# Kernel tuning notes

Hardware: AMD Instinct MI355X
Metric: run time of the kernel (lower is better)

The kernel has to match this reference:

```python
import jax, jax.numpy as jnp
import numpy as np

EPS = 1e-3  # Keras BatchNormalization default epsilon


def _bn_params(key, c):
    k1, k2, k3, k4 = jax.random.split(key, 4)
    gamma = 1.0 + 0.1 * jax.random.normal(k1, (c,), jnp.float32)
    beta = 0.1 * jax.random.normal(k2, (c,), jnp.float32)
    mean = 0.1 * jax.random.normal(k3, (c,), jnp.float32)
    var = 0.5 + jax.random.uniform(k4, (c,), jnp.float32)
    return jnp.stack([gamma, beta, mean, var])  # (4, c)


def bn(x, p):
    g, b, m, v = p[0], p[1], p[2], p[3]
    return (x - m) * jax.lax.rsqrt(v + EPS) * g + b


def setup_inputs() -> dict:
    key = jax.random.key(0)
    ks = jax.random.split(key, 32)
    B, N, C, K = 32, 2048, 3, 32
    MLP1, UNITS = 128, 512
    w = lambda k, shp, fan: jax.random.normal(k, shp, jnp.float32) / np.sqrt(fan)
    inp = {
        "inputs": jax.random.normal(ks[0], (B, N, C), jnp.float32),
        "indices": jax.random.randint(ks[1], (B, N, K), 0, N, jnp.int32),
        "t_conv1_w": w(ks[2], (C, 64), C), "t_conv1_b": 0.1 * jax.random.normal(ks[3], (64,), jnp.float32),
        "t_bn1": _bn_params(ks[4], 64),
        "t_dense1_w": w(ks[5], (64, 64), 64), "t_dense1_b": 0.1 * jax.random.normal(ks[6], (64,), jnp.float32),
        "t_bn2": _bn_params(ks[7], 64),
        "t_dense2_w": w(ks[8], (64, C * C), 64), "t_dense2_b": 0.1 * jax.random.normal(ks[9], (C * C,), jnp.float32),
        "conv1_w": w(ks[10], (K * C, MLP1), K * C), "conv1_b": 0.1 * jax.random.normal(ks[11], (MLP1,), jnp.float32),
        "bn1": _bn_params(ks[12], MLP1),
        "conv2_w": w(ks[13], (MLP1, 2 * MLP1), MLP1), "conv2_b": 0.1 * jax.random.normal(ks[14], (2 * MLP1,), jnp.float32),
        "bn2": _bn_params(ks[15], 2 * MLP1),
        "bn3": _bn_params(ks[16], 2 * MLP1),
        "dense1_w": w(ks[17], (2 * MLP1, C), 2 * MLP1), "dense1_b": 0.1 * jax.random.normal(ks[18], (C,), jnp.float32),
        "conv3_w": w(ks[19], (C, UNITS), C), "conv3_b": 0.1 * jax.random.normal(ks[20], (UNITS,), jnp.float32),
        "bn4": _bn_params(ks[21], UNITS),
        "blk1_w": w(ks[22], (UNITS, UNITS // 2), UNITS), "blk1_b": 0.1 * jax.random.normal(ks[23], (UNITS // 2,), jnp.float32),
        "blk1_bn": _bn_params(ks[24], UNITS // 2),
        "blk2_w": w(ks[25], (UNITS // 2, UNITS // 4), UNITS // 2), "blk2_b": 0.1 * jax.random.normal(ks[26], (UNITS // 4,), jnp.float32),
        "blk2_bn": _bn_params(ks[27], UNITS // 4),
        "bn_globf": _bn_params(ks[28], UNITS // 4),
    }
    return inp


def reference(inputs, indices, t_conv1_w, t_conv1_b, t_bn1, t_dense1_w, t_dense1_b,
              t_bn2, t_dense2_w, t_dense2_b, conv1_w, conv1_b, bn1, conv2_w, conv2_b,
              bn2, bn3, dense1_w, dense1_b, conv3_w, conv3_b, bn4,
              blk1_w, blk1_b, blk1_bn, blk2_w, blk2_b, blk2_bn, bn_globf):
    B, N, C = inputs.shape
    # --- TNetLess (inference: dropout = identity) ---
    x = jax.nn.relu(bn(inputs @ t_conv1_w + t_conv1_b, t_bn1))   # (B,N,64)
    x = jnp.max(x, axis=1)                                        # global max pool -> (B,64)
    x = jax.nn.relu(bn(x @ t_dense1_w + t_dense1_b, t_bn2))      # (B,64)
    transform = (x @ t_dense2_w + t_dense2_b).reshape(B, C, C)   # (B,C,C)
    pct = jnp.einsum('bnc,bcd->bnd', inputs, transform)          # transformed cloud (B,N,C)
    # --- random neighbor gather (batch_dims=1) ---
    feats = pct[jnp.arange(B)[:, None, None], indices]           # (B,N,K,C)
    feats = feats.reshape(B, N, -1)                               # (B,N,K*C)
    # --- pointwise MLP over gathered neighbor features ---
    feats = jax.nn.relu(bn(feats @ conv1_w + conv1_b, bn1))      # (B,N,128)
    feats = jax.nn.relu(bn(feats @ conv2_w + conv2_b, bn2))      # (B,N,256)
    g = bn(jnp.max(feats, axis=1), bn3)                           # (B,256)
    g = jnp.broadcast_to(g[:, None, :], (B, N, g.shape[-1]))     # tile to (B,N,256)
    g = g @ dense1_w + dense1_b                                   # (B,N,C)
    combined = jnp.concatenate([pct, g], axis=1)                  # concat on point axis -> (B,2N,C)
    # --- conv3 + conv blocks (kernel_size=1 -> pointwise) ---
    net = jax.nn.relu(bn(combined @ conv3_w + conv3_b, bn4))     # (B,2N,512)
    net = jax.nn.relu(bn(net @ blk1_w + blk1_b, blk1_bn))        # (B,2N,256)
    net = jax.nn.relu(bn(net @ blk2_w + blk2_b, blk2_bn))        # (B,2N,128)
    net = jnp.max(net, axis=1)                                    # (B,128)
    return bn(net, bn_globf)
```

## Files before the change

### kernel.cpp

```cpp
#include <hip/hip_runtime.h>

typedef unsigned short u16;
typedef unsigned int u32;
typedef __attribute__((ext_vector_type(8))) short bf16x8;
typedef __attribute__((ext_vector_type(4))) float f32x4;

#define EPSBN 0.001f
#define MFMA16(a, b, c) __builtin_amdgcn_mfma_f32_16x16x32_bf16(a, b, c, 0, 0, 0)

__device__ __forceinline__ float bf2f(u16 u) {
    return __uint_as_float(((u32)u) << 16);
}
__device__ __forceinline__ u16 f2bf(float f) {
    u32 u = __float_as_uint(f);
    u32 r = u + 0x7FFFu + ((u >> 16) & 1u);
    return (u16)(r >> 16);
}
__device__ __forceinline__ float relu(float x) { return x > 0.f ? x : 0.f; }
__device__ __forceinline__ float rdv(const void* p, int i, int isbf) {
    return isbf ? bf2f(((const u16*)p)[i]) : ((const float*)p)[i];
}

#define A_INPUTS 64
#define A_TC1W  196672
#define A_TC1B  196864
#define A_TBN1  196928
#define A_TD1W  197184
#define A_TD1B  201280
#define A_TBN2  201344
#define A_TD2W  201600
#define A_TD2B  202176
#define A_BN3   249216
#define A_D1W   250240
#define A_D1B   251008
#define A_BNGF  420928
#define S_PCT   423808
#define S_MAXF  620544
#define S_NETMAX 628736
#define T_C1WT  634880
#define T_C2WT  641024
#define T_W4T   657408
#define T_W5T   722944
#define P_W3S   739328
#define P_B3S   740864
#define P_BP1   741376
#define P_BP2   741504
#define P_BP4   741760
#define P_BP5   742016

struct SmallCv { const void* src[12]; int n[12]; int off[12]; };
struct PrepWA { const void* src[4]; const void* bn[4]; int K[4]; int logN[4]; int base[4]; int dstoff[4]; };
struct PrepSm { const void *bn4, *c3w, *c3b, *bn2, *c2b, *blk1bn, *blk1b, *bn1, *c1b, *blk2bn, *blk2b; };

__global__ __launch_bounds__(256) void k_prep(SmallCv sc, PrepWA pw, PrepSm ps,
                                              const void* __restrict__ inputs_raw,
                                              const u16* __restrict__ tbn1_raw,
                                              float* __restrict__ ws) {
    __shared__ float tile[32][65];
    __shared__ float scol[64];
    int isbf = 1;
    for (int i = 0; i < 16; i += 2) {
        u16 v = tbn1_raw[i];
        if (v < 0x3E00u || v > 0x4080u) isbf = 0;
    }
    int bx = blockIdx.x, tid = threadIdx.x;
    if (bx < 32) {
        float* dst = ws + A_INPUTS;
        for (int i = bx * 256 + tid; i < 196608; i += 8192) dst[i] = rdv(inputs_raw, i, isbf);
    } else if (bx < 36) {
        int t0 = (bx - 32) * 3;
        for (int t = t0; t < t0 + 3; t++) {
            int n = sc.n[t];
            float* dst = ws + sc.off[t];
            for (int i = tid; i < n; i += 256) dst[i] = rdv(sc.src[t], i, isbf);
        }
    } else if (bx < 138) {
        int blk = bx - 36;
        int t = (blk < 6) ? 0 : (blk < 22) ? 1 : (blk < 86) ? 2 : 3;
        int tt = blk - pw.base[t];
        int N = 1 << pw.logN[t];
        int K = pw.K[t];
        int ct = N >> 6;
        int k0 = (tt / ct) * 32, c0 = (tt % ct) * 64;
        if (tid < 64) {
            int c = c0 + tid;
            scol[tid] = rdv(pw.bn[t], c, isbf) * rsqrtf(rdv(pw.bn[t], 3 * N + c, isbf) + EPSBN);
        }
        __syncthreads();
#pragma unroll
        for (int pr = 0; pr < 8; pr++) {
            int kr = pr * 4 + (tid >> 6), cc = tid & 63;
            tile[kr][cc] = rdv(pw.src[t], (k0 + kr) * N + c0 + cc, isbf) * scol[cc];
        }
        __syncthreads();
        u32* d32 = (u32*)((u16*)(ws + pw.dstoff[t]));
#pragma unroll
        for (int pw2 = 0; pw2 < 4; pw2++) {
            int cr = pw2 * 16 + (tid >> 4);
            int kp = tid & 15;
            u32 pk = (u32)f2bf(tile[kp * 2][cr]) | ((u32)f2bf(tile[kp * 2 + 1][cr]) << 16);
            d32[(((c0 + cr) * K + k0) >> 1) + kp] = pk;
        }
    } else if (bx == 138) {
        for (int c = tid; c < 512; c += 256) {
            float s = rdv(ps.bn4, c, isbf) * rsqrtf(rdv(ps.bn4, 1536 + c, isbf) + EPSBN);
            float t = rdv(ps.bn4, 512 + c, isbf) - rdv(ps.bn4, 1024 + c, isbf) * s;
            ws[P_W3S + c]        = rdv(ps.c3w, c, isbf) * s;
            ws[P_W3S + 512 + c]  = rdv(ps.c3w, 512 + c, isbf) * s;
            ws[P_W3S + 1024 + c] = rdv(ps.c3w, 1024 + c, isbf) * s;
            ws[P_B3S + c] = rdv(ps.c3b, c, isbf) * s + t;
        }
        {
            int c = tid;
            float s2 = rdv(ps.bn2, c, isbf) * rsqrtf(rdv(ps.bn2, 768 + c, isbf) + EPSBN);
            ws[P_BP2 + c] = rdv(ps.c2b, c, isbf) * s2 + (rdv(ps.bn2, 256 + c, isbf) - rdv(ps.bn2, 512 + c, isbf) * s2);
            float s5 = rdv(ps.blk1bn, c, isbf) * rsqrtf(rdv(ps.blk1bn, 768 + c, isbf) + EPSBN);
            ws[P_BP4 + c] = rdv(ps.blk1b, c, isbf) * s5 + (rdv(ps.blk1bn, 256 + c, isbf) - rdv(ps.blk1bn, 512 + c, isbf) * s5);
        }
        if (tid < 128) {
            int c = tid;
            float s1 = rdv(ps.bn1, c, isbf) * rsqrtf(rdv(ps.bn1, 384 + c, isbf) + EPSBN);
            ws[P_BP1 + c] = rdv(ps.c1b, c, isbf) * s1 + (rdv(ps.bn1, 128 + c, isbf) - rdv(ps.bn1, 256 + c, isbf) * s1);
            float s6 = rdv(ps.blk2bn, c, isbf) * rsqrtf(rdv(ps.blk2bn, 384 + c, isbf) + EPSBN);
            ws[P_BP5 + c] = rdv(ps.blk2b, c, isbf) * s6 + (rdv(ps.blk2bn, 128 + c, isbf) - rdv(ps.blk2bn, 256 + c, isbf) * s6);
        }
    } else {
        u32* z = (u32*)(ws + S_MAXF);
        for (int i = tid; i < 12288; i += 256) z[i] = 0u;
        if (tid == 0) ((u32*)ws)[0] = (u32)isbf;
    }
}

__global__ __launch_bounds__(256) void k_tnet(const float* __restrict__ inp,
                                              const float* __restrict__ w,
                                              const float* __restrict__ bias,
                                              const float* __restrict__ bn,
                                              const float* __restrict__ w1, const float* __restrict__ b1,
                                              const float* __restrict__ bn2p,
                                              const float* __restrict__ w2, const float* __restrict__ b2,
                                              float* __restrict__ pct) {
    __shared__ float pts[6144];
    __shared__ float wred[4][64];
    __shared__ float x1v[64];
    __shared__ float x2v[64];
    __shared__ float tf[9];
    int b = blockIdx.x, tid = threadIdx.x;
    const float* ip = inp + (size_t)b * 2048 * 3;
#pragma unroll
    for (int i = 0; i < 24; i++) pts[tid + i * 256] = ip[tid + i * 256];

    int c = tid & 63, pg = tid >> 6;
    float w0 = w[c], w1c = w[64 + c], w2c = w[128 + c], bi = bias[c];
    float g = bn[c], be = bn[64 + c], m = bn[128 + c], v = bn[192 + c];
    float s = g * rsqrtf(v + EPSBN), t = be - m * s;
    __syncthreads();

    float vmax = 0.f;
    int pbase = pg * 512;
#pragma unroll 4
    for (int p = 0; p < 512; p++) {
        float x0 = pts[(pbase + p) * 3], x1 = pts[(pbase + p) * 3 + 1], x2 = pts[(pbase + p) * 3 + 2];
        float z = x0 * w0 + x1 * w1c + x2 * w2c + bi;
        vmax = fmaxf(vmax, z * s + t);
    }
    wred[pg][c] = vmax;
    __syncthreads();
    if (tid < 64) {
        float mm = fmaxf(fmaxf(wred[0][tid], wred[1][tid]), fmaxf(wred[2][tid], wred[3][tid]));
        x1v[tid] = relu(mm);
    }
    __syncthreads();
    if (tid < 64) {
        float acc = b1[tid];
        for (int j = 0; j < 64; j++) acc += x1v[j] * w1[j * 64 + tid];
        float g2 = bn2p[tid], be2 = bn2p[64 + tid], m2 = bn2p[128 + tid], v2 = bn2p[192 + tid];
        float s2 = g2 * rsqrtf(v2 + EPSBN);
        x2v[tid] = relu(acc * s2 + (be2 - m2 * s2));
    }
    __syncthreads();
    if (tid < 9) {
        float a = b2[tid];
        for (int j = 0; j < 64; j++) a += x2v[j] * w2[j * 9 + tid];
        tf[tid] = a;
    }
    __syncthreads();
    float t0 = tf[0], t1 = tf[1], t2 = tf[2], t3 = tf[3], t4 = tf[4];
    float t5 = tf[5], t6 = tf[6], t7 = tf[7], t8 = tf[8];
    float* op = pct + (size_t)b * 2048 * 3;
#pragma unroll
    for (int i = 0; i < 8; i++) {
        int p = tid + i * 256;
        float x0 = pts[p * 3], x1 = pts[p * 3 + 1], x2 = pts[p * 3 + 2];
        op[p * 3]     = x0 * t0 + x1 * t3 + x2 * t6;
        op[p * 3 + 1] = x0 * t1 + x1 * t4 + x2 * t7;
        op[p * 3 + 2] = x0 * t2 + x1 * t5 + x2 * t8;
    }
}

__global__ __launch_bounds__(256, 3) void k_featmlp(
    const float* __restrict__ pct, const int* __restrict__ indices,
    const u16* __restrict__ w1t, const float* __restrict__ bp1,
    const u16* __restrict__ w2t, const float* __restrict__ bp2,
    u32* __restrict__ maxfeats,
    const float* __restrict__ w3s, const float* __restrict__ b3s,
    const u16* __restrict__ w4t, const float* __restrict__ bp4,
    const u16* __restrict__ w5t, const float* __restrict__ bp5,
    u32* __restrict__ netmax) {
    __shared__ __align__(16) char SM[35328];
    int bx0 = blockIdx.x, tid = threadIdx.x;
    int bx = ((bx0 & 7) << 8) + (bx0 >> 3);
    int part = bx & 1;
    int idx = bx >> 1;
    int b = idx >> 5, sub = idx & 31;
    int lane = tid & 63, wv = tid >> 6;
    int rw = lane & 15, kq = lane >> 4;
    int axor = (rw & 7) << 4;

    if (part == 0) {
        char* ftA = SM;
        char* h1B = SM + 16384;
        float* sp1 = (float*)(SM + 32768);
        float* sp2 = (float*)(SM + 33280);
        int n0p = sub * 64;
        sp2[tid] = bp2[tid];
        if (tid < 128) sp1[tid] = bp1[tid];
        {
            const float* pb = pct + (size_t)b * 2048 * 3;
            const int* ib = indices + ((size_t)b * 2048 + n0p) * 32;
#pragma unroll
            for (int r = 0; r < 8; r++) {
                int i = tid + 256 * r;
                int p = i >> 5, k = i & 31;
                int idxp = ib[p * 32 + k];
                const float* s = pb + (size_t)idxp * 3;
                int sw = (p & 7) << 4;
                int base = p * 256 + 6 * k;
                *(u16*)(ftA + ((base) ^ sw))     = f2bf(s[0]);
                *(u16*)(ftA + ((base + 2) ^ sw)) = f2bf(s[1]);
                *(u16*)(ftA + ((base + 4) ^ sw)) = f2bf(s[2]);
            }
        }
        __syncthreads();
        {
            f32x4 acc[4][2];
#pragma unroll
            for (int m = 0; m < 4; m++)
#pragma unroll
                for (int n = 0; n < 2; n++) acc[m][n] = (f32x4){0.f, 0.f, 0.f, 0.f};
            const char* W = (const char*)w1t;
            int nb = wv * 32;
#pragma unroll
            for (int ks = 0; ks < 3; ks++) {
                int kb = ks * 64 + kq * 16;
                bf16x8 b0 = *(const bf16x8*)(W + (nb + rw) * 192 + kb);
                bf16x8 b1 = *(const bf16x8*)(W + (nb + 16 + rw) * 192 + kb);
                bf16x8 a0 = *(const bf16x8*)(ftA + (((rw) * 256 + kb) ^ axor));
                bf16x8 a1 = *(const bf16x8*)(ftA + (((rw + 16) * 256 + kb) ^ axor));
                bf16x8 a2 = *(const bf16x8*)(ftA + (((rw + 32) * 256 + kb) ^ axor));
                bf16x8 a3 = *(const bf16x8*)(ftA + (((rw + 48) * 256 + kb) ^ axor));
                acc[0][0] = MFMA16(a0, b0, acc[0][0]); acc[0][1] = MFMA16(a0, b1, acc[0][1]);
                acc[1][0] = MFMA16(a1, b0, acc[1][0]); acc[1][1] = MFMA16(a1, b1, acc[1][1]);
                acc[2][0] = MFMA16(a2, b0, acc[2][0]); acc[2][1] = MFMA16(a2, b1, acc[2][1]);
                acc[3][0] = MFMA16(a3, b0, acc[3][0]); acc[3][1] = MFMA16(a3, b1, acc[3][1]);
            }
#pragma unroll
            for (int nt = 0; nt < 2; nt++) {
                int c = nb + nt * 16 + rw;
                float bb = sp1[c];
#pragma unroll
                for (int m = 0; m < 4; m++)
#pragma unroll
                    for (int r = 0; r < 4; r++) {
                        int rr = m * 16 + kq * 4 + r;
                        float h = relu(acc[m][nt][r] + bb);
                        *(u16*)(h1B + ((rr * 256 + c * 2) ^ ((rr & 7) << 4))) = f2bf(h);
                    }
            }
        }
        __syncthreads();
        {
            f32x4 acc[4][4];
#pragma unroll
            for (int m = 0; m < 4; m++)
#pragma unroll
                for (int n = 0; n < 4; n++) acc[m][n] = (f32x4){0.f, 0.f, 0.f, 0.f};
            const char* W = (const char*)w2t;
            int nb = wv * 64;
#pragma unroll
            for (int ks = 0; ks < 4; ks++) {
                int kb = ks * 64 + kq * 16;
                bf16x8 a0 = *(const bf16x8*)(h1B + (((rw) * 256 + kb) ^ axor));
                bf16x8 a1 = *(const bf16x8*)(h1B + (((rw + 16) * 256 + kb) ^ axor));
                bf16x8 a2 = *(const bf16x8*)(h1B + (((rw + 32) * 256 + kb) ^ axor));
                bf16x8 a3 = *(const bf16x8*)(h1B + (((rw + 48) * 256 + kb) ^ axor));
#pragma unroll
                for (int nt = 0; nt < 4; nt++) {
                    bf16x8 bv = *(const bf16x8*)(W + (nb + nt * 16 + rw) * 256 + kb);
                    acc[0][nt] = MFMA16(a0, bv, acc[0][nt]);
                    acc[1][nt] = MFMA16(a1, bv, acc[1][nt]);
                    acc[2][nt] = MFMA16(a2, bv, acc[2][nt]);
                    acc[3][nt] = MFMA16(a3, bv, acc[3][nt]);
                }
            }
#pragma unroll
            for (int nt = 0; nt < 4; nt++) {
                int c = nb + nt * 16 + rw;
                float bb = sp2[c];
                float vm = 0.f;
#pragma unroll
                for (int m = 0; m < 4; m++)
#pragma unroll
                    for (int r = 0; r < 4; r++)
                        vm = fmaxf(vm, relu(acc[m][nt][r] + bb));
                vm = fmaxf(vm, __shfl_xor(vm, 16));
                vm = fmaxf(vm, __shfl_xor(vm, 32));
                if (kq == 0) atomicMax(&maxfeats[b * 256 + c], __float_as_uint(vm));
            }
        }
    } else {
        char* hA0 = SM;
        char* hA1 = SM + 8192;
        char* HB  = SM + 16384;
        float* rows4 = (float*)(SM + 32768);
        float* sb4 = (float*)(SM + 33792);
        float* sb5 = (float*)(SM + 34816);
        int r0 = sub * 64;

        sb4[tid] = bp4[tid];
        if (tid < 128) sb5[tid] = bp5[tid];
        if (tid < 64) {
            const float* s = pct + ((size_t)b * 2048 + r0 + tid) * 3;
            rows4[tid * 4] = s[0]; rows4[tid * 4 + 1] = s[1]; rows4[tid * 4 + 2] = s[2];
        }
        __syncthreads();

        auto phase1 = [&](int c, char* dst) {
            int c2 = (tid & 31) * 2;
            int rg = tid >> 5;
            int ch = c * 64 + c2;
            float wa0 = w3s[ch], wa1 = w3s[512 + ch], wa2 = w3s[1024 + ch], ba = b3s[ch];
            float wb0 = w3s[ch + 1], wb1 = w3s[513 + ch], wb2 = w3s[1025 + ch], bb2 = b3s[ch + 1];
#pragma unroll
            for (int r = 0; r < 8; r++) {
                int row = rg * 8 + r;
                float x0 = rows4[row * 4], x1 = rows4[row * 4 + 1], x2 = rows4[row * 4 + 2];
                float ha = relu(x0 * wa0 + x1 * wa1 + x2 * wa2 + ba);
                float hb = relu(x0 * wb0 + x1 * wb1 + x2 * wb2 + bb2);
                u32 pk = (u32)f2bf(ha) | ((u32)f2bf(hb) << 16);
                *(u32*)(dst + ((row * 128 + c2 * 2) ^ ((row & 7) << 4))) = pk;
            }
        };

        phase1(0, hA0);
        __syncthreads();

        f32x4 acc[4][4];
#pragma unroll
        for (int m = 0; m < 4; m++)
#pragma unroll
            for (int n = 0; n < 4; n++) acc[m][n] = (f32x4){0.f, 0.f, 0.f, 0.f};
        {
            const char* W = (const char*)w4t;
            int nb = wv * 64;
            for (int c = 0; c < 8; c++) {
                bf16x8 bfr[2][4];
#pragma unroll
                for (int ksl = 0; ksl < 2; ksl++)
#pragma unroll
                    for (int nt = 0; nt < 4; nt++)
                        bfr[ksl][nt] = *(const bf16x8*)(W + (nb + nt * 16 + rw) * 1024 + c * 128 + ksl * 64 + kq * 16);
                if (c < 7) phase1(c + 1, (c & 1) ? hA0 : hA1);
                const char* A = (c & 1) ? hA1 : hA0;
#pragma unroll
                for (int ksl = 0; ksl < 2; ksl++) {
                    int kb = ksl * 64 + kq * 16;
                    bf16x8 a0 = *(const bf16x8*)(A + (((rw) * 128 + kb) ^ axor));
                    bf16x8 a1 = *(const bf16x8*)(A + (((rw + 16) * 128 + kb) ^ axor));
                    bf16x8 a2 = *(const bf16x8*)(A + (((rw + 32) * 128 + kb) ^ axor));
                    bf16x8 a3 = *(const bf16x8*)(A + (((rw + 48) * 128 + kb) ^ axor));
#pragma unroll
                    for (int nt = 0; nt < 4; nt++) {
                        acc[0][nt] = MFMA16(a0, bfr[ksl][nt], acc[0][nt]);
                        acc[1][nt] = MFMA16(a1, bfr[ksl][nt], acc[1][nt]);
                        acc[2][nt] = MFMA16(a2, bfr[ksl][nt], acc[2][nt]);
                        acc[3][nt] = MFMA16(a3, bfr[ksl][nt], acc[3][nt]);
                    }
                }
                __syncthreads();
            }
        }
        float vm[2] = {0.f, 0.f};
        const char* W5 = (const char*)w5t;
        int nb2 = wv * 32;
#pragma unroll
        for (int h = 0; h < 2; h++) {
#pragma unroll
            for (int nt = 0; nt < 4; nt++) {
                int c = wv * 64 + nt * 16 + rw;
                float bb = sb4[c];
#pragma unroll
                for (int m = 0; m < 2; m++) {
                    int mm = h * 2 + m;
#pragma unroll
                    for (int r = 0; r < 4; r++) {
                        int rr = m * 16 + kq * 4 + r;
                        float hh = relu(acc[mm][nt][r] + bb);
                        *(u16*)(HB + ((rr * 512 + c * 2) ^ ((rr & 7) << 4))) = f2bf(hh);
                    }
                }
            }
            __syncthreads();
            f32x4 acc3[2][2];
#pragma unroll
            for (int m = 0; m < 2; m++)
#pragma unroll
                for (int n = 0; n < 2; n++) acc3[m][n] = (f32x4){0.f, 0.f, 0.f, 0.f};
#pragma unroll
            for (int ks = 0; ks < 8; ks++) {
                int kb = ks * 64 + kq * 16;
                bf16x8 b0 = *(const bf16x8*)(W5 + (nb2 + rw) * 512 + kb);
                bf16x8 b1 = *(const bf16x8*)(W5 + (nb2 + 16 + rw) * 512 + kb);
                bf16x8 a0 = *(const bf16x8*)(HB + (((rw) * 512 + kb) ^ axor));
                bf16x8 a1 = *(const bf16x8*)(HB + (((rw + 16) * 512 + kb) ^ axor));
                acc3[0][0] = MFMA16(a0, b0, acc3[0][0]); acc3[0][1] = MFMA16(a0, b1, acc3[0][1]);
                acc3[1][0] = MFMA16(a1, b0, acc3[1][0]); acc3[1][1] = MFMA16(a1, b1, acc3[1][1]);
            }
#pragma unroll
            for (int nt = 0; nt < 2; nt++) {
                int c = nb2 + nt * 16 + rw;
                float bb = sb5[c];
#pragma unroll
                for (int m = 0; m < 2; m++)
#pragma unroll
                    for (int r = 0; r < 4; r++)
                        vm[nt] = fmaxf(vm[nt], relu(acc3[m][nt][r] + bb));
            }
            __syncthreads();
        }
#pragma unroll
        for (int nt = 0; nt < 2; nt++) {
            int c = nb2 + nt * 16 + rw;
            float v = vm[nt];
            v = fmaxf(v, __shfl_xor(v, 16));
            v = fmaxf(v, __shfl_xor(v, 32));
            if (kq == 0) atomicMax(&netmax[b * 128 + c], __float_as_uint(v));
        }
    }
}

__global__ __launch_bounds__(256) void k_gtail(const u32* __restrict__ maxfeats,
                                               const float* __restrict__ bn3p,
                                               const float* __restrict__ dw, const float* __restrict__ db,
                                               const float* __restrict__ w3s, const float* __restrict__ b3s,
                                               const u16* __restrict__ w4t, const float* __restrict__ bp4,
                                               const u16* __restrict__ w5t, const float* __restrict__ bp5,
                                               u32* __restrict__ netmax,
                                               const float* __restrict__ bng,
                                               const u32* __restrict__ flag,
                                               void* __restrict__ out) {
    __shared__ float red[3][256];
    __shared__ float h512[512];
    __shared__ float h256[256];
    __shared__ float gv[4];
    int b = blockIdx.x, c = threadIdx.x;
    float mf = __uint_as_float(maxfeats[b * 256 + c]);
    float g = bn3p[c], be = bn3p[256 + c], m = bn3p[512 + c], v = bn3p[768 + c];
    float s = g * rsqrtf(v + EPSBN);
    float y = mf * s + (be - m * s);
    red[0][c] = y * dw[c * 3 + 0];
    red[1][c] = y * dw[c * 3 + 1];
    red[2][c] = y * dw[c * 3 + 2];
    __syncthreads();
    for (int st = 128; st > 0; st >>= 1) {
        if (c < st) {
            red[0][c] += red[0][c + st];
            red[1][c] += red[1][c + st];
            red[2][c] += red[2][c + st];
        }
        __syncthreads();
    }
    if (c < 3) gv[c] = red[c][0] + db[c];
    __syncthreads();
    float g0 = gv[0], g1 = gv[1], g2 = gv[2];
    for (int h = c; h < 512; h += 256)
        h512[h] = relu(g0 * w3s[h] + g1 * w3s[512 + h] + g2 * w3s[1024 + h] + b3s[h]);
    __syncthreads();
    {
        float acc = 0.f;
        const bf16x8* wr = (const bf16x8*)(w4t + (size_t)c * 512);
        for (int i = 0; i < 64; i++) {
            bf16x8 vv = wr[i];
#pragma unroll
            for (int j = 0; j < 8; j++) acc += h512[i * 8 + j] * bf2f((u16)vv[j]);
        }
        h256[c] = relu(acc + bp4[c]);
    }
    __syncthreads();
    if (c < 128) {
        float acc = 0.f;
        const bf16x8* wr = (const bf16x8*)(w5t + (size_t)c * 256);
        for (int i = 0; i < 32; i++) {
            bf16x8 vv = wr[i];
#pragma unroll
            for (int j = 0; j < 8; j++) acc += h256[i * 8 + j] * bf2f((u16)vv[j]);
        }
        u32 mybits = __float_as_uint(relu(acc + bp5[c]));
        u32 old = atomicMax(&netmax[b * 128 + c], mybits);
        u32 fin = old > mybits ? old : mybits;
        float vv = __uint_as_float(fin);
        float gg = bng[c], bee = bng[128 + c], mm = bng[256 + c], va = bng[384 + c];
        float ss = gg * rsqrtf(va + EPSBN);
        float val = vv * ss + (bee - mm * ss);
        int oi = b * 128 + c;
        if (flag[0]) ((u16*)out)[oi] = f2bf(val);
        else ((float*)out)[oi] = val;
    }
}

extern "C" void kernel_launch(void* const* d_in, const int* in_sizes, int n_in,
                              void* d_out, int out_size, void* d_ws, size_t ws_size,
                              hipStream_t stream) {
    float* ws = (float*)d_ws;
    const int* indices = (const int*)d_in[1];

    SmallCv sc;
    {
        static const int srcix[12] = {2, 3, 4, 5, 6, 7, 8, 9, 16, 17, 18, 28};
        static const int nels[12] = {192, 64, 256, 4096, 64, 256, 576, 9, 1024, 768, 3, 512};
        static const int offs[12] = {A_TC1W, A_TC1B, A_TBN1, A_TD1W, A_TD1B, A_TBN2, A_TD2W, A_TD2B,
                                     A_BN3, A_D1W, A_D1B, A_BNGF};
        for (int i = 0; i < 12; i++) { sc.src[i] = d_in[srcix[i]]; sc.n[i] = nels[i]; sc.off[i] = offs[i]; }
    }
    PrepWA pw;
    pw.src[0] = d_in[10]; pw.bn[0] = d_in[12]; pw.K[0] = 96;  pw.logN[0] = 7; pw.base[0] = 0;  pw.dstoff[0] = T_C1WT;
    pw.src[1] = d_in[13]; pw.bn[1] = d_in[15]; pw.K[1] = 128; pw.logN[1] = 8; pw.base[1] = 6;  pw.dstoff[1] = T_C2WT;
    pw.src[2] = d_in[22]; pw.bn[2] = d_in[24]; pw.K[2] = 512; pw.logN[2] = 8; pw.base[2] = 22; pw.dstoff[2] = T_W4T;
    pw.src[3] = d_in[25]; pw.bn[3] = d_in[27]; pw.K[3] = 256; pw.logN[3] = 7; pw.base[3] = 86; pw.dstoff[3] = T_W5T;
    PrepSm ps;
    ps.bn4 = d_in[21]; ps.c3w = d_in[19]; ps.c3b = d_in[20];
    ps.bn2 = d_in[15]; ps.c2b = d_in[14];
    ps.blk1bn = d_in[24]; ps.blk1b = d_in[23];
    ps.bn1 = d_in[12]; ps.c1b = d_in[11];
    ps.blk2bn = d_in[27]; ps.blk2b = d_in[26];

    k_prep<<<140, 256, 0, stream>>>(sc, pw, ps, d_in[0], (const u16*)d_in[4], ws);

    k_tnet<<<32, 256, 0, stream>>>(ws + A_INPUTS, ws + A_TC1W, ws + A_TC1B, ws + A_TBN1,
                                   ws + A_TD1W, ws + A_TD1B, ws + A_TBN2,
                                   ws + A_TD2W, ws + A_TD2B, ws + S_PCT);

    k_featmlp<<<2048, 256, 0, stream>>>(ws + S_PCT, indices,
                                        (const u16*)(ws + T_C1WT), ws + P_BP1,
                                        (const u16*)(ws + T_C2WT), ws + P_BP2,
                                        (u32*)(ws + S_MAXF),
                                        ws + P_W3S, ws + P_B3S,
                                        (const u16*)(ws + T_W4T), ws + P_BP4,
                                        (const u16*)(ws + T_W5T), ws + P_BP5,
                                        (u32*)(ws + S_NETMAX));

    k_gtail<<<32, 256, 0, stream>>>((u32*)(ws + S_MAXF), ws + A_BN3, ws + A_D1W, ws + A_D1B,
                                    ws + P_W3S, ws + P_B3S,
                                    (const u16*)(ws + T_W4T), ws + P_BP4,
                                    (const u16*)(ws + T_W5T), ws + P_BP5,
                                    (u32*)(ws + S_NETMAX),
                                    ws + A_BNGF, (u32*)ws, d_out);
}
```

Before: 268.0 us.

## Split T-Net max pass across point slices and software-pipeline weight loads

The T-Net first stage is split into a kernel that runs 8 point slices per batch and merges per-channel maxima with atomicMax into a zeroed workspace buffer, followed by a small kernel that finishes the dense layers and applies the transform. This raises parallelism from 32 blocks to 256 for the point-wise max pass, at the cost of one extra launch and a round trip through global memory. Separately, the featmlp GEMM loops now prefetch the next k-step's weight fragments into registers before issuing the current MFMAs, to hide global or cache load latency. The prefetching adds register pressure, which could hurt occupancy at the declared launch bounds.

Measured after the change: 247.8 us. 1.08x faster.

```diff
diff --git a/kernel.cpp b/kernel.cpp
--- a/kernel.cpp
+++ b/kernel.cpp
@@ -37,6 +37,7 @@
 #define S_PCT   423808
 #define S_MAXF  620544
 #define S_NETMAX 628736
+#define S_XMAX  632832
 #define T_C1WT  634880
 #define T_C2WT  641024
 #define T_W4T   657408
@@ -126,49 +127,57 @@
         }
     } else {
         u32* z = (u32*)(ws + S_MAXF);
-        for (int i = tid; i < 12288; i += 256) z[i] = 0u;
+        for (int i = tid; i < 14336; i += 256) z[i] = 0u;
         if (tid == 0) ((u32*)ws)[0] = (u32)isbf;
     }
 }
 
-__global__ __launch_bounds__(256) void k_tnet(const float* __restrict__ inp,
-                                              const float* __restrict__ w,
-                                              const float* __restrict__ bias,
-                                              const float* __restrict__ bn,
-                                              const float* __restrict__ w1, const float* __restrict__ b1,
-                                              const float* __restrict__ bn2p,
-                                              const float* __restrict__ w2, const float* __restrict__ b2,
-                                              float* __restrict__ pct) {
-    __shared__ float pts[6144];
+__global__ __launch_bounds__(256) void k_tnet1(const float* __restrict__ inp,
+                                               const float* __restrict__ w,
+                                               const float* __restrict__ bias,
+                                               const float* __restrict__ bn,
+                                               u32* __restrict__ xmax) {
+    __shared__ float pts[768];
     __shared__ float wred[4][64];
+    int b = blockIdx.y, slice = blockIdx.x, tid = threadIdx.x;
+    const float* ip = inp + ((size_t)b * 2048 + slice * 256) * 3;
+    pts[tid] = ip[tid];
+    pts[tid + 256] = ip[tid + 256];
+    pts[tid + 512] = ip[tid + 512];
+
+    int c = tid & 63, np = tid >> 6;
+    float w0 = w[c], w1c = w[64 + c], w2c = w[128 + c], bi = bias[c];
+    float g = bn[c], be = bn[64 + c], m = bn[128 + c], v = bn[192 + c];
+    float s = g * rsqrtf(v + EPSBN), t = be - m * s;
+    __syncthreads();
+
+    float vmax = -1e30f;
+    int pbase = np * 64;
+#pragma unroll 4
+    for (int p = 0; p < 64; p++) {
+        float x0 = pts[(pbase + p) * 3], x1 = pts[(pbase + p) * 3 + 1], x2 = pts[(pbase + p) * 3 + 2];
+        float z = x0 * w0 + x1 * w1c + x2 * w2c + bi;
+        vmax = fmaxf(vmax, z * s + t);
+    }
+    wred[np][c] = vmax;
+    __syncthreads();
+    if (tid < 64) {
+        float mm = fmaxf(fmaxf(wred[0][tid], wred[1][tid]), fmaxf(wred[2][tid], wred[3][tid]));
+        atomicMax(&xmax[b * 64 + tid], __float_as_uint(relu(mm)));
+    }
+}
+
+__global__ __launch_bounds__(256) void k_tnet2pct(const float* __restrict__ inp,
+                                                  const u32* __restrict__ xmax,
+                                                  const float* __restrict__ w1, const float* __restrict__ b1,
+                                                  const float* __restrict__ bn2p,
+                                                  const float* __restrict__ w2, const float* __restrict__ b2,
+                                                  float* __restrict__ pct) {
     __shared__ float x1v[64];
     __shared__ float x2v[64];
     __shared__ float tf[9];
     int b = blockIdx.x, tid = threadIdx.x;
-    const float* ip = inp + (size_t)b * 2048 * 3;
-#pragma unroll
-    for (int i = 0; i < 24; i++) pts[tid + i * 256] = ip[tid + i * 256];
-
-    int c = tid & 63, pg = tid >> 6;
-    float w0 = w[c], w1c = w[64 + c], w2c = w[128 + c], bi = bias[c];
-    float g = bn[c], be = bn[64 + c], m = bn[128 + c], v = bn[192 + c];
-    float s = g * rsqrtf(v + EPSBN), t = be - m * s;
-    __syncthreads();
-
-    float vmax = 0.f;
-    int pbase = pg * 512;
-#pragma unroll 4
-    for (int p = 0; p < 512; p++) {
-        float x0 = pts[(pbase + p) * 3], x1 = pts[(pbase + p) * 3 + 1], x2 = pts[(pbase + p) * 3 + 2];
-        float z = x0 * w0 + x1 * w1c + x2 * w2c + bi;
-        vmax = fmaxf(vmax, z * s + t);
-    }
-    wred[pg][c] = vmax;
-    __syncthreads();
-    if (tid < 64) {
-        float mm = fmaxf(fmaxf(wred[0][tid], wred[1][tid]), fmaxf(wred[2][tid], wred[3][tid]));
-        x1v[tid] = relu(mm);
-    }
+    if (tid < 64) x1v[tid] = __uint_as_float(xmax[b * 64 + tid]);
     __syncthreads();
     if (tid < 64) {
         float acc = b1[tid];
@@ -186,11 +195,12 @@
     __syncthreads();
     float t0 = tf[0], t1 = tf[1], t2 = tf[2], t3 = tf[3], t4 = tf[4];
     float t5 = tf[5], t6 = tf[6], t7 = tf[7], t8 = tf[8];
+    const float* ip = inp + (size_t)b * 2048 * 3;
     float* op = pct + (size_t)b * 2048 * 3;
 #pragma unroll
     for (int i = 0; i < 8; i++) {
         int p = tid + i * 256;
-        float x0 = pts[p * 3], x1 = pts[p * 3 + 1], x2 = pts[p * 3 + 2];
+        float x0 = ip[p * 3], x1 = ip[p * 3 + 1], x2 = ip[p * 3 + 2];
         op[p * 3]     = x0 * t0 + x1 * t3 + x2 * t6;
         op[p * 3 + 1] = x0 * t1 + x1 * t4 + x2 * t7;
         op[p * 3 + 2] = x0 * t2 + x1 * t5 + x2 * t8;
@@ -286,6 +296,10 @@
                 for (int n = 0; n < 4; n++) acc[m][n] = (f32x4){0.f, 0.f, 0.f, 0.f};
             const char* W = (const char*)w2t;
             int nb = wv * 64;
+            bf16x8 p0 = *(const bf16x8*)(W + (nb + rw) * 256 + kq * 16);
+            bf16x8 p1 = *(const bf16x8*)(W + (nb + 16 + rw) * 256 + kq * 16);
+            bf16x8 p2 = *(const bf16x8*)(W + (nb + 32 + rw) * 256 + kq * 16);
+            bf16x8 p3 = *(const bf16x8*)(W + (nb + 48 + rw) * 256 + kq * 16);
 #pragma unroll
             for (int ks = 0; ks < 4; ks++) {
                 int kb = ks * 64 + kq * 16;
@@ -293,14 +307,22 @@
                 bf16x8 a1 = *(const bf16x8*)(h1B + (((rw + 16) * 256 + kb) ^ axor));
                 bf16x8 a2 = *(const bf16x8*)(h1B + (((rw + 32) * 256 + kb) ^ axor));
                 bf16x8 a3 = *(const bf16x8*)(h1B + (((rw + 48) * 256 + kb) ^ axor));
-#pragma unroll
-                for (int nt = 0; nt < 4; nt++) {
-                    bf16x8 bv = *(const bf16x8*)(W + (nb + nt * 16 + rw) * 256 + kb);
-                    acc[0][nt] = MFMA16(a0, bv, acc[0][nt]);
-                    acc[1][nt] = MFMA16(a1, bv, acc[1][nt]);
-                    acc[2][nt] = MFMA16(a2, bv, acc[2][nt]);
-                    acc[3][nt] = MFMA16(a3, bv, acc[3][nt]);
+                bf16x8 b0 = p0, b1 = p1, b2 = p2, b3 = p3;
+                if (ks < 3) {
+                    int kn = (ks + 1) * 64 + kq * 16;
+                    p0 = *(const bf16x8*)(W + (nb + rw) * 256 + kn);
+                    p1 = *(const bf16x8*)(W + (nb + 16 + rw) * 256 + kn);
+                    p2 = *(const bf16x8*)(W + (nb + 32 + rw) * 256 + kn);
+                    p3 = *(const bf16x8*)(W + (nb + 48 + rw) * 256 + kn);
                 }
+                acc[0][0] = MFMA16(a0, b0, acc[0][0]); acc[1][0] = MFMA16(a1, b0, acc[1][0]);
+                acc[2][0] = MFMA16(a2, b0, acc[2][0]); acc[3][0] = MFMA16(a3, b0, acc[3][0]);
+                acc[0][1] = MFMA16(a0, b1, acc[0][1]); acc[1][1] = MFMA16(a1, b1, acc[1][1]);
+                acc[2][1] = MFMA16(a2, b1, acc[2][1]); acc[3][1] = MFMA16(a3, b1, acc[3][1]);
+                acc[0][2] = MFMA16(a0, b2, acc[0][2]); acc[1][2] = MFMA16(a1, b2, acc[1][2]);
+                acc[2][2] = MFMA16(a2, b2, acc[2][2]); acc[3][2] = MFMA16(a3, b2, acc[3][2]);
+                acc[0][3] = MFMA16(a0, b3, acc[0][3]); acc[1][3] = MFMA16(a1, b3, acc[1][3]);
+                acc[2][3] = MFMA16(a2, b3, acc[2][3]); acc[3][3] = MFMA16(a3, b3, acc[3][3]);
             }
 #pragma unroll
             for (int nt = 0; nt < 4; nt++) {
@@ -362,29 +384,44 @@
         {
             const char* W = (const char*)w4t;
             int nb = wv * 64;
+            auto ldB = [&](int c, int ksl, int nt) -> bf16x8 {
+                return *(const bf16x8*)(W + (nb + nt * 16 + rw) * 1024 + c * 128 + ksl * 64 + kq * 16);
+            };
+            bf16x8 pf0 = ldB(0, 0, 0), pf1 = ldB(0, 0, 1), pf2 = ldB(0, 0, 2), pf3 = ldB(0, 0, 3);
             for (int c = 0; c < 8; c++) {
-                bf16x8 bfr[2][4];
-#pragma unroll
-                for (int ksl = 0; ksl < 2; ksl++)
-#pragma unroll
-                    for (int nt = 0; nt < 4; nt++)
-                        bfr[ksl][nt] = *(const bf16x8*)(W + (nb + nt * 16 + rw) * 1024 + c * 128 + ksl * 64 + kq * 16);
+                bf16x8 q0 = ldB(c, 1, 0), q1 = ldB(c, 1, 1), q2 = ldB(c, 1, 2), q3 = ldB(c, 1, 3);
                 if (c < 7) phase1(c + 1, (c & 1) ? hA0 : hA1);
                 const char* A = (c & 1) ? hA1 : hA0;
-#pragma unroll
-                for (int ksl = 0; ksl < 2; ksl++) {
-                    int kb = ksl * 64 + kq * 16;
+                {
+                    int kb = kq * 16;
                     bf16x8 a0 = *(const bf16x8*)(A + (((rw) * 128 + kb) ^ axor));
                     bf16x8 a1 = *(const bf16x8*)(A + (((rw + 16) * 128 + kb) ^ axor));
                     bf16x8 a2 = *(const bf16x8*)(A + (((rw + 32) * 128 + kb) ^ axor));
                     bf16x8 a3 = *(const bf16x8*)(A + (((rw + 48) * 128 + kb) ^ axor));
-#pragma unroll
-                    for (int nt = 0; nt < 4; nt++) {
-                        acc[0][nt] = MFMA16(a0, bfr[ksl][nt], acc[0][nt]);
-                        acc[1][nt] = MFMA16(a1, bfr[ksl][nt], acc[1][nt]);
-                        acc[2][nt] = MFMA16(a2, bfr[ksl][nt], acc[2][nt]);
-                        acc[3][nt] = MFMA16(a3, bfr[ksl][nt], acc[3][nt]);
-                    }
+                    acc[0][0] = MFMA16(a0, pf0, acc[0][0]); acc[1][0] = MFMA16(a1, pf0, acc[1][0]);
+                    acc[2][0] = MFMA16(a2, pf0, acc[2][0]); acc[3][0] = MFMA16(a3, pf0, acc[3][0]);
+                    acc[0][1] = MFMA16(a0, pf1, acc[0][1]); acc[1][1] = MFMA16(a1, pf1, acc[1][1]);
+                    acc[2][1] = MFMA16(a2, pf1, acc[2][1]); acc[3][1] = MFMA16(a3, pf1, acc[3][1]);
+                    acc[0][2] = MFMA16(a0, pf2, acc[0][2]); acc[1][2] = MFMA16(a1, pf2, acc[1][2]);
+                    acc[2][2] = MFMA16(a2, pf2, acc[2][2]); acc[3][2] = MFMA16(a3, pf2, acc[3][2]);
+                    acc[0][3] = MFMA16(a0, pf3, acc[0][3]); acc[1][3] = MFMA16(a1, pf3, acc[1][3]);
+                    acc[2][3] = MFMA16(a2, pf3, acc[2][3]); acc[3][3] = MFMA16(a3, pf3, acc[3][3]);
+                }
+                if (c < 7) { pf0 = ldB(c + 1, 0, 0); pf1 = ldB(c + 1, 0, 1); pf2 = ldB(c + 1, 0, 2); pf3 = ldB(c + 1, 0, 3); }
+                {
+                    int kb = 64 + kq * 16;
+                    bf16x8 a0 = *(const bf16x8*)(A + (((rw) * 128 + kb) ^ axor));
+                    bf16x8 a1 = *(const bf16x8*)(A + (((rw + 16) * 128 + kb) ^ axor));
+                    bf16x8 a2 = *(const bf16x8*)(A + (((rw + 32) * 128 + kb) ^ axor));
+                    bf16x8 a3 = *(const bf16x8*)(A + (((rw + 48) * 128 + kb) ^ axor));
+                    acc[0][0] = MFMA16(a0, q0, acc[0][0]); acc[1][0] = MFMA16(a1, q0, acc[1][0]);
+                    acc[2][0] = MFMA16(a2, q0, acc[2][0]); acc[3][0] = MFMA16(a3, q0, acc[3][0]);
+                    acc[0][1] = MFMA16(a0, q1, acc[0][1]); acc[1][1] = MFMA16(a1, q1, acc[1][1]);
+                    acc[2][1] = MFMA16(a2, q1, acc[2][1]); acc[3][1] = MFMA16(a3, q1, acc[3][1]);
+                    acc[0][2] = MFMA16(a0, q2, acc[0][2]); acc[1][2] = MFMA16(a1, q2, acc[1][2]);
+                    acc[2][2] = MFMA16(a2, q2, acc[2][2]); acc[3][2] = MFMA16(a3, q2, acc[3][2]);
+                    acc[0][3] = MFMA16(a0, q3, acc[0][3]); acc[1][3] = MFMA16(a1, q3, acc[1][3]);
+                    acc[2][3] = MFMA16(a2, q3, acc[2][3]); acc[3][3] = MFMA16(a3, q3, acc[3][3]);
                 }
                 __syncthreads();
             }
@@ -415,13 +452,19 @@
             for (int m = 0; m < 2; m++)
 #pragma unroll
                 for (int n = 0; n < 2; n++) acc3[m][n] = (f32x4){0.f, 0.f, 0.f, 0.f};
+            bf16x8 pb0 = *(const bf16x8*)(W5 + (nb2 + rw) * 512 + kq * 16);
+            bf16x8 pb1 = *(const bf16x8*)(W5 + (nb2 + 16 + rw) * 512 + kq * 16);
 #pragma unroll
             for (int ks = 0; ks < 8; ks++) {
                 int kb = ks * 64 + kq * 16;
-                bf16x8 b0 = *(const bf16x8*)(W5 + (nb2 + rw) * 512 + kb);
-                bf16x8 b1 = *(const bf16x8*)(W5 + (nb2 + 16 + rw) * 512 + kb);
+                bf16x8 b0 = pb0, b1 = pb1;
                 bf16x8 a0 = *(const bf16x8*)(HB + (((rw) * 512 + kb) ^ axor));
                 bf16x8 a1 = *(const bf16x8*)(HB + (((rw + 16) * 512 + kb) ^ axor));
+                if (ks < 7) {
+                    int kn = (ks + 1) * 64 + kq * 16;
+                    pb0 = *(const bf16x8*)(W5 + (nb2 + rw) * 512 + kn);
+                    pb1 = *(const bf16x8*)(W5 + (nb2 + 16 + rw) * 512 + kn);
+                }
                 acc3[0][0] = MFMA16(a0, b0, acc3[0][0]); acc3[0][1] = MFMA16(a0, b1, acc3[0][1]);
                 acc3[1][0] = MFMA16(a1, b0, acc3[1][0]); acc3[1][1] = MFMA16(a1, b1, acc3[1][1]);
             }
@@ -545,9 +588,11 @@
 
     k_prep<<<140, 256, 0, stream>>>(sc, pw, ps, d_in[0], (const u16*)d_in[4], ws);
 
-    k_tnet<<<32, 256, 0, stream>>>(ws + A_INPUTS, ws + A_TC1W, ws + A_TC1B, ws + A_TBN1,
-                                   ws + A_TD1W, ws + A_TD1B, ws + A_TBN2,
-                                   ws + A_TD2W, ws + A_TD2B, ws + S_PCT);
+    k_tnet1<<<dim3(8, 32), 256, 0, stream>>>(ws + A_INPUTS, ws + A_TC1W, ws + A_TC1B, ws + A_TBN1,
+                                             (u32*)(ws + S_XMAX));
+    k_tnet2pct<<<32, 256, 0, stream>>>(ws + A_INPUTS, (const u32*)(ws + S_XMAX),
+                                       ws + A_TD1W, ws + A_TD1B, ws + A_TBN2,
+                                       ws + A_TD2W, ws + A_TD2B, ws + S_PCT);
 
     k_featmlp<<<2048, 256, 0, stream>>>(ws + S_PCT, indices,
                                         (const u16*)(ws + T_C1WT), ws + P_BP1,
```
